# Kernel optimization log

Measured on AMD Instinct MI355X. Metric: run time of the kernel, lower is better.

## Reference

```python
import jax, jax.numpy as jnp
import numpy as np

B, N, D, H, O, A, L = 128, 100, 2048, 1024, 1600, 400, 2048


def _mlp(x, w1, b1, w2, b2, w3, b3):
    h = jax.nn.relu(x @ w1 + b1)
    h = jax.nn.relu(h @ w2 + b2)
    return jax.nn.softmax(h @ w3 + b3, axis=2)  # softmax over class dim (dim=2)


def setup_inputs() -> dict:
    key = jax.random.key(0)
    ks = jax.random.split(key, 18)

    def lin(kw, fan_in, fan_out):
        s = 1.0 / np.sqrt(fan_in)
        return jax.random.normal(kw, (fan_in, fan_out), jnp.float32) * s

    x = jax.random.normal(ks[0], (B, N, D), jnp.float32)
    num_descs = jax.random.randint(ks[1], (B,), 0, N, jnp.int32)
    label_img = jnp.sort(jax.random.randint(ks[2], (L,), 0, B, jnp.int32))
    obj_labels = jax.random.randint(ks[3], (L,), 0, O)
    att_labels = jax.random.randint(ks[4], (L,), 0, A)

    inp = dict(x=x, num_descs=num_descs, label_img=label_img,
               obj_labels=obj_labels, att_labels=att_labels,
               w1o=lin(ks[5], D, H), b1o=jnp.zeros((H,), jnp.float32),
               w2o=lin(ks[6], H, H), b2o=jnp.zeros((H,), jnp.float32),
               w3o=lin(ks[7], H, O), b3o=jnp.zeros((O,), jnp.float32),
               w1a=lin(ks[8], D, H), b1a=jnp.zeros((H,), jnp.float32),
               w2a=lin(ks[9], H, H), b2a=jnp.zeros((H,), jnp.float32),
               w3a=lin(ks[10], H, A), b3a=jnp.zeros((A,), jnp.float32))
    return inp


def reference(x, num_descs, label_img, obj_labels, att_labels,
              w1o, b1o, w2o, b2o, w3o, b3o,
              w1a, b1a, w2a, b2a, w3a, b3a):
    po = _mlp(x, w1o, b1o, w2o, b2o, w3o, b3o)  # [B, N, O]
    pa = _mlp(x, w1a, b1a, w2a, b2a, w3a, b3a)  # [B, N, A]

    rows = jnp.arange(po.shape[1])  # [N]
    # per-label gather of the prob column for its object/attribute class -> [L, N]
    p_obj = po[label_img[:, None], rows[None, :], obj_labels[:, None]]
    p_att = pa[label_img[:, None], rows[None, :], att_labels[:, None]]
    # ragged unpad (descs beyond num_descs[img] excluded from argmax)
    valid = rows[None, :] < num_descs[label_img][:, None]
    score = jnp.where(valid, p_obj * p_att, -jnp.inf)
    desc = jnp.argmax(score, axis=1)  # [L]

    obj_dists = po[label_img, desc, :]  # [L, O]
    att_dists = pa[label_img, desc, :]  # [L, A]
    return (obj_dists, att_dists)
```

## Files before the change

kernel.cpp:

```cpp
#include <hip/hip_runtime.h>
#include <hip/hip_bf16.h>
#include <math.h>

#define Bq 128
#define Nq 100
#define Dq 2048
#define Hq 1024
#define Oq 1600
#define Aq 400
#define Lq 2048
#define Mq (Bq * Nq)
#define OqP 1664
#define AqP 512

typedef __attribute__((ext_vector_type(8))) short bf16x8;
typedef __attribute__((ext_vector_type(16))) float f32x16;
typedef unsigned short ushort;


__device__ __forceinline__ void split1(float v, ushort& h, ushort& l) {
    __hip_bfloat16 bh = __float2bfloat16(v);
    float fh = __bfloat162float(bh);
    __hip_bfloat16 bl = __float2bfloat16(v - fh);
    h = __builtin_bit_cast(ushort, bh);
    l = __builtin_bit_cast(ushort, bl);
}

__device__ __forceinline__ void gl_lds16(const ushort* g, ushort* lds) {
    __builtin_amdgcn_global_load_lds(
        (const __attribute__((address_space(1))) unsigned int*)g,
        (__attribute__((address_space(3))) unsigned int*)lds,
        16, 0, 0);
}

__global__ void build_offsets(const int* __restrict__ num_descs,
                              int* __restrict__ off, int* __restrict__ mc,
                              int* __restrict__ rowmap)
{
    __shared__ int cnt[Bq];
    __shared__ int offs[Bq + 1];
    const int t = threadIdx.x;
    int nd = num_descs[t];
    nd = nd < 0 ? 0 : (nd > Nq ? Nq : nd);
    const int c = nd < 1 ? 1 : nd;
    cnt[t] = c;
    __syncthreads();
    if (t == 0) {
        int s = 0;
        for (int i = 0; i < Bq; i++) { offs[i] = s; s += cnt[i]; }
        offs[Bq] = s;
        mc[0] = s;
        mc[1] = (s + 127) & ~127;
    }
    __syncthreads();
    off[t] = offs[t];
    for (int i = t; i < Mq; i += Bq) rowmap[i] = -1;
    __syncthreads();
    const int o = offs[t];
    for (int n = 0; n < c; n++) rowmap[o + n] = t * Nq + n;
}

__global__ void split_compact(const float* __restrict__ x,
                              const int* __restrict__ rowmap,
                              const int* __restrict__ mc,
                              ushort* __restrict__ hi, ushort* __restrict__ lo)
{
    const int KB = Dq / 16;
    const int wid = (blockIdx.x * blockDim.x + threadIdx.x) >> 6;
    const int lane = threadIdx.x & 63;
    const int rt = wid / KB;
    const int kb = wid - rt * KB;
    if (rt * 32 >= mc[1]) return;
    const int crow = rt * 32 + (lane & 31);
    const int k = kb * 16 + (lane >> 5) * 8;
    const int orig = (crow < mc[0]) ? rowmap[crow] : -1;
    ushort h[8], l[8];
    if (orig < 0) {
#pragma unroll
        for (int j = 0; j < 8; j++) { h[j] = 0; l[j] = 0; }
    } else {
        const float* src = x + (size_t)orig * Dq + k;
        float4 v0 = *(const float4*)(src);
        float4 v1 = *(const float4*)(src + 4);
        float v[8] = {v0.x, v0.y, v0.z, v0.w, v1.x, v1.y, v1.z, v1.w};
#pragma unroll
        for (int j = 0; j < 8; j++) split1(v[j], h[j], l[j]);
    }
    const size_t a = (size_t)wid * 512 + (size_t)lane * 8;
    *(bf16x8*)(hi + a) = *(bf16x8*)h;
    *(bf16x8*)(lo + a) = *(bf16x8*)l;
}

struct TSeg { const float* W; ushort* Th; ushort* Tl; int K; int N; int gx; int base; };
struct TSegs { TSeg s[6]; };

__global__ void tsplit_all(TSegs a)
{
    const int id = blockIdx.x;
    TSeg sg = a.s[5];
#pragma unroll
    for (int i = 4; i >= 0; i--) if (id < a.s[i + 1].base) sg = a.s[i];
    const int local = id - sg.base;
    const int bn = (local % sg.gx) * 32;
    const int bk = (local / sg.gx) * 32;
    const int KB = sg.K >> 4;

    __shared__ float t[32][33];
    const int tx = threadIdx.x & 31, ty = threadIdx.x >> 5;
#pragma unroll
    for (int i = 0; i < 4; i++) {
        const int k = bk + ty + i * 8, n = bn + tx;
        t[ty + i * 8][tx] = (n < sg.N) ? sg.W[(size_t)k * sg.N + n] : 0.f;
    }
    __syncthreads();

    const int wave = threadIdx.x >> 6;
    const int lane = threadIdx.x & 63;
    const int kc = wave & 1;
    const int hl = wave >> 1;
    const int nloc = lane & 31;
    const int kloc = kc * 16 + (lane >> 5) * 8;
    ushort v8[8];
#pragma unroll
    for (int e = 0; e < 8; e++) {
        ushort h, l;
        split1(t[kloc + e][nloc], h, l);
        v8[e] = hl ? l : h;
    }
    const size_t chunk = (size_t)((bn >> 5)) * KB + (bk >> 4) + kc;
    ushort* dst = (hl ? sg.Tl : sg.Th) + chunk * 512 + (size_t)lane * 8;
    *(bf16x8*)dst = *(bf16x8*)v8;
}

struct GArgs {
    const ushort* Ah; const ushort* Al;
    const ushort* Bh; const ushort* Bl;
    const float* bias;
    float* Cf; ushort* Ch; ushort* Cl;
    int K, Npad, Nreal, ldc, mode;
};

__global__ __launch_bounds__(256) void gemm_split(GArgs g0, GArgs g1,
                                                  const int* __restrict__ mcp)
{
    const GArgs g = (blockIdx.z == 0) ? g0 : g1;
    const int bm = blockIdx.y * 128;
    const int bn = blockIdx.x * 128;
    if (bn >= g.Npad) return;
    if (bm >= mcp[1]) return;

    const int KB = g.K >> 4;

    __shared__ __align__(16) ushort sAh[4096];
    __shared__ __align__(16) ushort sAl[4096];
    __shared__ __align__(16) ushort sBh[4096];
    __shared__ __align__(16) ushort sBl[4096];

    const int tid  = threadIdx.x;
    const int wave = tid >> 6;
    const int lane = tid & 63;
    const int wmi = (wave >> 1) * 2;
    const int wni = (wave & 1) * 2;
    const int l31  = lane & 31;
    const int half = lane >> 5;

    const ushort* gAh = g.Ah + ((size_t)(bm / 32 + wave) * KB) * 512 + lane * 8;
    const ushort* gAl = g.Al + ((size_t)(bm / 32 + wave) * KB) * 512 + lane * 8;
    const ushort* gBh = g.Bh + ((size_t)(bn / 32 + wave) * KB) * 512 + lane * 8;
    const ushort* gBl = g.Bl + ((size_t)(bn / 32 + wave) * KB) * 512 + lane * 8;
    ushort* lAh = &sAh[wave * 1024];
    ushort* lAl = &sAl[wave * 1024];
    ushort* lBh = &sBh[wave * 1024];
    ushort* lBl = &sBl[wave * 1024];

    f32x16 acc[2][2] = {};

    for (int kc = 0; kc < KB; kc += 2) {
        const size_t go = (size_t)kc * 512;
        gl_lds16(gAh + go, lAh);  gl_lds16(gAh + go + 512, lAh + 512);
        gl_lds16(gAl + go, lAl);  gl_lds16(gAl + go + 512, lAl + 512);
        gl_lds16(gBh + go, lBh);  gl_lds16(gBh + go + 512, lBh + 512);
        gl_lds16(gBl + go, lBl);  gl_lds16(gBl + go + 512, lBl + 512);
        __syncthreads();

#pragma unroll
        for (int ks = 0; ks < 2; ks++) {
            bf16x8 ah[2], al[2], bh[2], bl[2];
#pragma unroll
            for (int i = 0; i < 2; i++) {
                const int sa = ((wmi + i) * 2 + ks) * 512 + lane * 8;
                const int sb = ((wni + i) * 2 + ks) * 512 + lane * 8;
                ah[i] = *(const bf16x8*)&sAh[sa];
                al[i] = *(const bf16x8*)&sAl[sa];
                bh[i] = *(const bf16x8*)&sBh[sb];
                bl[i] = *(const bf16x8*)&sBl[sb];
            }
#pragma unroll
            for (int i = 0; i < 2; i++)
#pragma unroll
                for (int j = 0; j < 2; j++) {
                    acc[i][j] = __builtin_amdgcn_mfma_f32_32x32x16_bf16(ah[i], bh[j], acc[i][j], 0, 0, 0);
                    acc[i][j] = __builtin_amdgcn_mfma_f32_32x32x16_bf16(ah[i], bl[j], acc[i][j], 0, 0, 0);
                    acc[i][j] = __builtin_amdgcn_mfma_f32_32x32x16_bf16(al[i], bh[j], acc[i][j], 0, 0, 0);
                }
        }
        __syncthreads();
    }

    const int KC = g.ldc >> 4;
#pragma unroll
    for (int j = 0; j < 2; j++) {
        const int col = bn + (wni + j) * 32 + l31;
        if (col < g.Nreal) {
            const float bv = g.bias[col];
#pragma unroll
            for (int i = 0; i < 2; i++) {
#pragma unroll
                for (int r = 0; r < 16; r++) {
                    const int row = bm + (wmi + i) * 32 + (r & 3) + 8 * (r >> 2) + 4 * half;
                    float v = acc[i][j][r] + bv;
                    if (g.mode == 1) {
                        v = fmaxf(v, 0.f);
                        ushort h, l;
                        split1(v, h, l);
                        const size_t chunk = (size_t)(row >> 5) * KC + (col >> 4);
                        const size_t adr = chunk * 512
                            + (size_t)((row & 31) + 32 * ((col >> 3) & 1)) * 8 + (col & 7);
                        g.Ch[adr] = h;
                        g.Cl[adr] = l;
                    } else {
                        g.Cf[(size_t)row * g.ldc + col] = v;
                    }
                }
            }
        }
    }
}

__global__ void softmax_stats2(const float* __restrict__ Zo, const float* __restrict__ Za,
                               const int* __restrict__ mc,
                               float* __restrict__ mxo, float* __restrict__ smo,
                               float* __restrict__ mxa, float* __restrict__ sma)
{
    const int r = blockIdx.x;
    if (r >= mc[0]) return;
    const float* Z; int ncols; float* mx; float* sm;
    if (blockIdx.y == 0) { Z = Zo; ncols = Oq; mx = mxo; sm = smo; }
    else                 { Z = Za; ncols = Aq; mx = mxa; sm = sma; }
    const float* row = Z + (size_t)r * ncols;
    __shared__ float red[256];
    float m = -INFINITY;
    for (int c = threadIdx.x; c < ncols; c += 256) m = fmaxf(m, row[c]);
    red[threadIdx.x] = m;
    __syncthreads();
    for (int s = 128; s > 0; s >>= 1) {
        if (threadIdx.x < s) red[threadIdx.x] = fmaxf(red[threadIdx.x], red[threadIdx.x + s]);
        __syncthreads();
    }
    m = red[0];
    __syncthreads();
    float su = 0.f;
    for (int c = threadIdx.x; c < ncols; c += 256) su += expf(row[c] - m);
    red[threadIdx.x] = su;
    __syncthreads();
    for (int s = 128; s > 0; s >>= 1) {
        if (threadIdx.x < s) red[threadIdx.x] += red[threadIdx.x + s];
        __syncthreads();
    }
    if (threadIdx.x == 0) { mx[r] = m; sm[r] = red[0]; }
}

__global__ void argmax_gather(
    const float* __restrict__ Zo, const float* __restrict__ Za,
    const float* __restrict__ mxo, const float* __restrict__ smo,
    const float* __restrict__ mxa, const float* __restrict__ sma,
    const int* __restrict__ label_img, const int* __restrict__ num_descs,
    const int* __restrict__ obj_labels, const int* __restrict__ att_labels,
    const int* __restrict__ off, float* __restrict__ out)
{
    const int l = blockIdx.x;
    const int b = label_img[l];
    const int nd = num_descs[b];
    const int r0 = off[b];
    const int t = threadIdx.x;

    __shared__ float ss[128];
    __shared__ int   si[128];
    if (t < 128) {
        float score = -INFINITY;
        if (t < Nq && t < nd) {
            const int r = r0 + t;
            const float po = expf(Zo[(size_t)r * Oq + obj_labels[l]] - mxo[r]) / smo[r];
            const float pa = expf(Za[(size_t)r * Aq + att_labels[l]] - mxa[r]) / sma[r];
            score = po * pa;
        }
        ss[t] = score;
        si[t] = t;
    }
    __syncthreads();
    for (int s = 64; s > 0; s >>= 1) {
        if (t < s) {
            const float s2 = ss[t + s];
            const int   i2 = si[t + s];
            if (s2 > ss[t] || (s2 == ss[t] && i2 < si[t])) { ss[t] = s2; si[t] = i2; }
        }
        __syncthreads();
    }
    const int r = r0 + si[0];

    const float mo = mxo[r], so = smo[r];
    const float* zo = Zo + (size_t)r * Oq;
    float* oo = out + (size_t)l * Oq;
    for (int c = t; c < Oq; c += 256)
        oo[c] = expf(zo[c] - mo) / so;

    const float ma = mxa[r], sa = sma[r];
    const float* za = Za + (size_t)r * Aq;
    float* oa = out + (size_t)Lq * Oq + (size_t)l * Aq;
    for (int c = t; c < Aq; c += 256)
        oa[c] = expf(za[c] - ma) / sa;
}

extern "C" void kernel_launch(void* const* d_in, const int* in_sizes, int n_in,
                              void* d_out, int out_size, void* d_ws, size_t ws_size,
                              hipStream_t stream)
{
    const float* x          = (const float*)d_in[0];
    const int*   num_descs  = (const int*)d_in[1];
    const int*   label_img  = (const int*)d_in[2];
    const int*   obj_labels = (const int*)d_in[3];
    const int*   att_labels = (const int*)d_in[4];
    const float* w1o = (const float*)d_in[5];  const float* b1o = (const float*)d_in[6];
    const float* w2o = (const float*)d_in[7];  const float* b2o = (const float*)d_in[8];
    const float* w3o = (const float*)d_in[9];  const float* b3o = (const float*)d_in[10];
    const float* w1a = (const float*)d_in[11]; const float* b1a = (const float*)d_in[12];
    const float* w2a = (const float*)d_in[13]; const float* b2a = (const float*)d_in[14];
    const float* w3a = (const float*)d_in[15]; const float* b3a = (const float*)d_in[16];
    float* out = (float*)d_out;

    char* p = (char*)d_ws;
    auto carve = [&](size_t bytes) { char* q = p; p += (bytes + 255) & ~(size_t)255; return q; };

    char* bufA = carve((size_t)Mq * Dq * 2 * 2);
    char* bufB = carve((size_t)Mq * Hq * 2 * 2 * 2);
    ushort* w1oth = (ushort*)carve((size_t)Hq * Dq * 2);  ushort* w1otl = (ushort*)carve((size_t)Hq * Dq * 2);
    ushort* w1ath = (ushort*)carve((size_t)Hq * Dq * 2);  ushort* w1atl = (ushort*)carve((size_t)Hq * Dq * 2);
    ushort* w2oth = (ushort*)carve((size_t)Hq * Hq * 2);  ushort* w2otl = (ushort*)carve((size_t)Hq * Hq * 2);
    ushort* w2ath = (ushort*)carve((size_t)Hq * Hq * 2);  ushort* w2atl = (ushort*)carve((size_t)Hq * Hq * 2);
    ushort* w3oth = (ushort*)carve((size_t)OqP * Hq * 2); ushort* w3otl = (ushort*)carve((size_t)OqP * Hq * 2);
    ushort* w3ath = (ushort*)carve((size_t)AqP * Hq * 2); ushort* w3atl = (ushort*)carve((size_t)AqP * Hq * 2);
    float* mxo = (float*)carve(Mq * 4); float* smo = (float*)carve(Mq * 4);
    float* mxa = (float*)carve(Mq * 4); float* sma = (float*)carve(Mq * 4);
    int* off    = (int*)carve(Bq * 4);
    int* mc     = (int*)carve(2 * 4);
    int* rowmap = (int*)carve(Mq * 4);

    ushort* xh = (ushort*)bufA;
    ushort* xl = xh + (size_t)Mq * Dq;
    ushort* h2oh = (ushort*)bufA;
    ushort* h2ol = h2oh + (size_t)Mq * Hq;
    ushort* h2ah = h2ol + (size_t)Mq * Hq;
    ushort* h2al = h2ah + (size_t)Mq * Hq;
    ushort* h1oh = (ushort*)bufB;
    ushort* h1ol = h1oh + (size_t)Mq * Hq;
    ushort* h1ah = h1ol + (size_t)Mq * Hq;
    ushort* h1al = h1ah + (size_t)Mq * Hq;
    float* z3o = (float*)bufB;
    float* z3a = z3o + (size_t)Mq * Oq;

    build_offsets<<<1, 128, 0, stream>>>(num_descs, off, mc, rowmap);
    split_compact<<<(Mq / 32) * (Dq / 16) / 4, 256, 0, stream>>>(x, rowmap, mc, xh, xl);

    {
        TSegs ts;
        int base = 0;
        auto seg = [&](const float* W, ushort* Th, ushort* Tl, int K, int N, int Npad) {
            TSeg s; s.W = W; s.Th = Th; s.Tl = Tl; s.K = K; s.N = N;
            s.gx = Npad / 32; s.base = base; base += (Npad / 32) * (K / 32); return s;
        };
        ts.s[0] = seg(w1o, w1oth, w1otl, Dq, Hq, Hq);
        ts.s[1] = seg(w1a, w1ath, w1atl, Dq, Hq, Hq);
        ts.s[2] = seg(w2o, w2oth, w2otl, Hq, Hq, Hq);
        ts.s[3] = seg(w2a, w2ath, w2atl, Hq, Hq, Hq);
        ts.s[4] = seg(w3o, w3oth, w3otl, Hq, Oq, OqP);
        ts.s[5] = seg(w3a, w3ath, w3atl, Hq, Aq, AqP);
        tsplit_all<<<base, 256, 0, stream>>>(ts);
    }

    {
        GArgs go = { xh, xl, w1oth, w1otl, b1o, nullptr, h1oh, h1ol, Dq, Hq, Hq, Hq, 1 };
        GArgs ga = { xh, xl, w1ath, w1atl, b1a, nullptr, h1ah, h1al, Dq, Hq, Hq, Hq, 1 };
        gemm_split<<<dim3(Hq / 128, Mq / 128, 2), 256, 0, stream>>>(go, ga, mc);
    }
    {
        GArgs go = { h1oh, h1ol, w2oth, w2otl, b2o, nullptr, h2oh, h2ol, Hq, Hq, Hq, Hq, 1 };
        GArgs ga = { h1ah, h1al, w2ath, w2atl, b2a, nullptr, h2ah, h2al, Hq, Hq, Hq, Hq, 1 };
        gemm_split<<<dim3(Hq / 128, Mq / 128, 2), 256, 0, stream>>>(go, ga, mc);
    }
    {
        GArgs go = { h2oh, h2ol, w3oth, w3otl, b3o, z3o, nullptr, nullptr, Hq, OqP, Oq, Oq, 0 };
        GArgs ga = { h2ah, h2al, w3ath, w3atl, b3a, z3a, nullptr, nullptr, Hq, AqP, Aq, Aq, 0 };
        gemm_split<<<dim3(OqP / 128, Mq / 128, 2), 256, 0, stream>>>(go, ga, mc);
    }

    softmax_stats2<<<dim3(Mq, 2), 256, 0, stream>>>(z3o, z3a, mc, mxo, smo, mxa, sma);
    argmax_gather<<<Lq, 256, 0, stream>>>(z3o, z3a, mxo, smo, mxa, sma,
                                          label_img, num_descs, obj_labels, att_labels, off, out);
}
```

Measured before the change: 657.4 us.

## Add 4-slot LDS ring pipeline with async prefetch and MFMA priority to split GEMM

Replaces the load-sync-compute-sync loop with a 4-slot shared-memory ring. Global-to-LDS loads for chunk c+3 are issued while chunk c is computed, and explicit vmcnt waits plus one barrier per phase replace the two __syncthreads per iteration. It also raises wave priority around the MFMA block and adds launch_bounds(256,2). LDS use doubles to 64KB per block, which may limit occupancy, and the hand-placed waitcnt/barrier logic must be exactly right to avoid races.

Measured after the change: 600.1 us. 1.1x faster.

```diff
diff --git a/kernel.cpp b/kernel.cpp
--- a/kernel.cpp
+++ b/kernel.cpp
@@ -140,8 +140,8 @@
     int K, Npad, Nreal, ldc, mode;
 };
 
-__global__ __launch_bounds__(256) void gemm_split(GArgs g0, GArgs g1,
-                                                  const int* __restrict__ mcp)
+__global__ __launch_bounds__(256, 2) void gemm_split(GArgs g0, GArgs g1,
+                                                     const int* __restrict__ mcp)
 {
     const GArgs g = (blockIdx.z == 0) ? g0 : g1;
     const int bm = blockIdx.y * 128;
@@ -151,10 +151,10 @@
 
     const int KB = g.K >> 4;
 
-    __shared__ __align__(16) ushort sAh[4096];
-    __shared__ __align__(16) ushort sAl[4096];
-    __shared__ __align__(16) ushort sBh[4096];
-    __shared__ __align__(16) ushort sBl[4096];
+    __shared__ __align__(16) ushort sAh[8192];
+    __shared__ __align__(16) ushort sAl[8192];
+    __shared__ __align__(16) ushort sBh[8192];
+    __shared__ __align__(16) ushort sBl[8192];
 
     const int tid  = threadIdx.x;
     const int wave = tid >> 6;
@@ -168,44 +168,58 @@
     const ushort* gAl = g.Al + ((size_t)(bm / 32 + wave) * KB) * 512 + lane * 8;
     const ushort* gBh = g.Bh + ((size_t)(bn / 32 + wave) * KB) * 512 + lane * 8;
     const ushort* gBl = g.Bl + ((size_t)(bn / 32 + wave) * KB) * 512 + lane * 8;
-    ushort* lAh = &sAh[wave * 1024];
-    ushort* lAl = &sAl[wave * 1024];
-    ushort* lBh = &sBh[wave * 1024];
-    ushort* lBl = &sBl[wave * 1024];
 
     f32x16 acc[2][2] = {};
 
-    for (int kc = 0; kc < KB; kc += 2) {
-        const size_t go = (size_t)kc * 512;
-        gl_lds16(gAh + go, lAh);  gl_lds16(gAh + go + 512, lAh + 512);
-        gl_lds16(gAl + go, lAl);  gl_lds16(gAl + go + 512, lAl + 512);
-        gl_lds16(gBh + go, lBh);  gl_lds16(gBh + go + 512, lBh + 512);
-        gl_lds16(gBl + go, lBl);  gl_lds16(gBl + go + 512, lBl + 512);
-        __syncthreads();
-
-#pragma unroll
-        for (int ks = 0; ks < 2; ks++) {
-            bf16x8 ah[2], al[2], bh[2], bl[2];
-#pragma unroll
-            for (int i = 0; i < 2; i++) {
-                const int sa = ((wmi + i) * 2 + ks) * 512 + lane * 8;
-                const int sb = ((wni + i) * 2 + ks) * 512 + lane * 8;
-                ah[i] = *(const bf16x8*)&sAh[sa];
-                al[i] = *(const bf16x8*)&sAl[sa];
-                bh[i] = *(const bf16x8*)&sBh[sb];
-                bl[i] = *(const bf16x8*)&sBl[sb];
+    auto STAGE = [&](int c) {
+        const size_t go = (size_t)c * 512;
+        const int ls = ((c & 3) << 11) + (wave << 9);
+        gl_lds16(gAh + go, &sAh[ls]);
+        gl_lds16(gAl + go, &sAl[ls]);
+        gl_lds16(gBh + go, &sBh[ls]);
+        gl_lds16(gBl + go, &sBl[ls]);
+    };
+
+    auto PHASE = [&](int c, int stage_c, int drain) {
+        const int slot = (c & 3) << 11;
+        bf16x8 ah[2], al[2], bh[2], bl[2];
+#pragma unroll
+        for (int i = 0; i < 2; i++) {
+            const int sa = slot + (wmi + i) * 512 + lane * 8;
+            const int sb = slot + (wni + i) * 512 + lane * 8;
+            ah[i] = *(const bf16x8*)&sAh[sa];
+            al[i] = *(const bf16x8*)&sAl[sa];
+            bh[i] = *(const bf16x8*)&sBh[sb];
+            bl[i] = *(const bf16x8*)&sBl[sb];
+        }
+        if (stage_c >= 0) STAGE(stage_c);
+        asm volatile("s_waitcnt lgkmcnt(0)" ::: "memory");
+        __builtin_amdgcn_sched_barrier(0);
+        __builtin_amdgcn_s_setprio(1);
+#pragma unroll
+        for (int i = 0; i < 2; i++)
+#pragma unroll
+            for (int j = 0; j < 2; j++) {
+                acc[i][j] = __builtin_amdgcn_mfma_f32_32x32x16_bf16(ah[i], bh[j], acc[i][j], 0, 0, 0);
+                acc[i][j] = __builtin_amdgcn_mfma_f32_32x32x16_bf16(ah[i], bl[j], acc[i][j], 0, 0, 0);
+                acc[i][j] = __builtin_amdgcn_mfma_f32_32x32x16_bf16(al[i], bh[j], acc[i][j], 0, 0, 0);
             }
-#pragma unroll
-            for (int i = 0; i < 2; i++)
-#pragma unroll
-                for (int j = 0; j < 2; j++) {
-                    acc[i][j] = __builtin_amdgcn_mfma_f32_32x32x16_bf16(ah[i], bh[j], acc[i][j], 0, 0, 0);
-                    acc[i][j] = __builtin_amdgcn_mfma_f32_32x32x16_bf16(ah[i], bl[j], acc[i][j], 0, 0, 0);
-                    acc[i][j] = __builtin_amdgcn_mfma_f32_32x32x16_bf16(al[i], bh[j], acc[i][j], 0, 0, 0);
-                }
-        }
-        __syncthreads();
-    }
+        __builtin_amdgcn_s_setprio(0);
+        __builtin_amdgcn_sched_barrier(0);
+        if (drain == 8)      asm volatile("s_waitcnt vmcnt(8)" ::: "memory");
+        else if (drain == 4) asm volatile("s_waitcnt vmcnt(4)" ::: "memory");
+        else if (drain == 0) asm volatile("s_waitcnt vmcnt(0)" ::: "memory");
+        if (drain >= 0)      asm volatile("s_barrier" ::: "memory");
+    };
+
+    STAGE(0); STAGE(1); STAGE(2);
+    asm volatile("s_waitcnt vmcnt(8)" ::: "memory");
+    asm volatile("s_barrier" ::: "memory");
+
+    for (int c = 0; c < KB - 3; ++c) PHASE(c, c + 3, 8);
+    PHASE(KB - 3, -1, 4);
+    PHASE(KB - 2, -1, 0);
+    PHASE(KB - 1, -1, -1);
 
     const int KC = g.ldc >> 4;
 #pragma unroll
```
